# Kernel optimization log

Hardware: AMD Instinct MI355X
Metric: run time of the kernel (lower is better)

## Reference

```python
import jax, jax.numpy as jnp
import numpy as np

B, T, S, I, H = 128, 256, 256, 512, 512


def setup_inputs() -> dict:
    key = jax.random.key(0)
    ks = jax.random.split(key, 10)
    sc = 0.02
    return {
        "x": jax.random.normal(ks[0], (B, T, I), jnp.float32),
        "h0": jax.random.normal(ks[1], (B, H), jnp.float32),
        "c0": jax.random.normal(ks[2], (B, H), jnp.float32),
        "ctx": jax.random.normal(ks[3], (S, B, H), jnp.float32),
        "Wi": jax.random.normal(ks[4], (4 * H, I), jnp.float32) * sc,
        "bi": jax.random.normal(ks[5], (4 * H,), jnp.float32) * sc,
        "Wh": jax.random.normal(ks[6], (4 * H, H), jnp.float32) * sc,
        "bh": jax.random.normal(ks[7], (4 * H,), jnp.float32) * sc,
        "W_in": jax.random.normal(ks[8], (H, H), jnp.float32) * sc,
        "W_out": jax.random.normal(ks[9], (H, 2 * H), jnp.float32) * sc,
    }


def reference(x, h0, c0, ctx, Wi, bi, Wh, bh, W_in, W_out):
    ctx_b = jnp.transpose(ctx, (1, 0, 2))  # [B, S, H]

    def step(carry, xt):
        hx, cx = carry
        gates = xt @ Wi.T + bi + hx @ Wh.T + bh  # [B, 4H]
        i_g, f_g, g_g, o_g = jnp.split(gates, 4, axis=1)
        cy = jax.nn.sigmoid(f_g) * cx + jax.nn.sigmoid(i_g) * jnp.tanh(g_g)
        hy = jax.nn.sigmoid(o_g) * jnp.tanh(cy)
        # soft dot attention
        target = hy @ W_in.T                              # [B, H]
        attn = jax.nn.softmax(jnp.einsum('bsh,bh->bs', ctx_b, target), axis=1)
        wc = jnp.einsum('bs,bsh->bh', attn, ctx_b)        # [B, H]
        h_tilde = jnp.tanh(jnp.concatenate([wc, hy], axis=1) @ W_out.T)
        return (h_tilde, cy), h_tilde

    (hf, cf), outs = jax.lax.scan(step, (h0, c0), jnp.transpose(x, (1, 0, 2)))
    output = jnp.transpose(outs, (1, 0, 2))  # [B, T, H] (batch_first)
    return output, hf, cf
```

## Files before the change

kernel.cpp:

```cpp
#include <hip/hip_runtime.h>
#include <hip/hip_bf16.h>
#include <stdint.h>

#define B_ 128
#define T_ 256
#define S_ 256
#define I_ 512
#define H_ 512
#define RSLOT 32

typedef __attribute__((ext_vector_type(8))) short short8;
typedef __attribute__((ext_vector_type(4))) float f32x4;
typedef unsigned short ushort_t;
typedef unsigned long long u64;

__device__ __forceinline__ float bf2f(ushort_t u){
  union{ unsigned int i; float f;} v; v.i = ((unsigned int)u)<<16; return v.f;
}
__device__ __forceinline__ ushort_t f2bf(float f){
  union{ unsigned int i; float f;} v; v.f=f;
  unsigned int x=v.i; unsigned int r = x + 0x7fffu + ((x>>16)&1u);
  return (ushort_t)(r>>16);
}
__device__ __forceinline__ float sigm(float x){ return 1.f/(1.f + __expf(-x)); }
__device__ __forceinline__ float tanh_s(float x){
  float a = fabsf(x);
  float e = __expf(-2.f*a);
  float t = (1.f - e)/(1.f + e);
  return x < 0.f ? -t : t;
}

__device__ __forceinline__ f32x4 MFMA16(short8 a, short8 b, f32x4 c){
  typedef __attribute__((ext_vector_type(8))) __bf16 bf16x8;
  return __builtin_amdgcn_mfma_f32_16x16x32_bf16(
      __builtin_bit_cast(bf16x8, a), __builtin_bit_cast(bf16x8, b), c, 0, 0, 0);
}

__device__ __forceinline__ void fab_store_u64(void* p, u64 v){
  __hip_atomic_store((u64*)p, v, __ATOMIC_RELAXED, __HIP_MEMORY_SCOPE_AGENT);
}


__global__ void k_cvt_bf16(const float* __restrict__ src, ushort_t* __restrict__ dst, int n){
  int i = (blockIdx.x*blockDim.x + threadIdx.x)*4;
  int stride = gridDim.x*blockDim.x*4;
  for (; i < n; i += stride){
    float4 v = *(const float4*)(src + i);
    ushort4 o; o.x=f2bf(v.x); o.y=f2bf(v.y); o.z=f2bf(v.z); o.w=f2bf(v.w);
    *(ushort4*)(dst + i) = o;
  }
}

__global__ void k_init_state(const float* __restrict__ h0, const float* __restrict__ c0,
                             ushort_t* __restrict__ hring0, float* __restrict__ cyb){
  int i = blockIdx.x*blockDim.x + threadIdx.x;
  hring0[i] = f2bf(h0[i]);
  cyb[i] = c0[i];
}

__global__ void k_zero_bar(int* f){
  f[threadIdx.x] = 0;
}

__global__ __launch_bounds__(256) void k_gemm_bt(
    const float* __restrict__ A, const float* __restrict__ Bm,
    ushort_t* __restrict__ C, int M, int N, int K,
    const float* __restrict__ bias0, const float* __restrict__ bias1){
  __shared__ ushort_t Asm[128][40];
  __shared__ ushort_t Bsm[128][40];
  const int tid = threadIdx.x;
  const int mBase = blockIdx.x*128, nBase = blockIdx.y*128;
  const int l = tid & 63, wv = tid >> 6;
  const int wm = (wv>>1)*64, wn = (wv&1)*64;
  const int lr = l & 15, lq = l >> 4;
  const int srow = tid >> 1, scol = (tid & 1)*16;
  const float* Ap = A + (size_t)(mBase + srow)*K + scol;
  const float* Bp = Bm + (size_t)(nBase + srow)*K + scol;

  f32x4 acc[4][4];
  #pragma unroll
  for (int i=0;i<4;i++)
    #pragma unroll
    for (int j=0;j<4;j++) acc[i][j] = (f32x4)0.f;

  for (int k0 = 0; k0 < K; k0 += 32){
    float4 a0 = *(const float4*)(Ap + k0);
    float4 a1 = *(const float4*)(Ap + k0 + 4);
    float4 a2 = *(const float4*)(Ap + k0 + 8);
    float4 a3 = *(const float4*)(Ap + k0 + 12);
    float4 b0 = *(const float4*)(Bp + k0);
    float4 b1 = *(const float4*)(Bp + k0 + 4);
    float4 b2 = *(const float4*)(Bp + k0 + 8);
    float4 b3 = *(const float4*)(Bp + k0 + 12);
    __syncthreads();
    {
      ushort4 w;
      w.x=f2bf(a0.x); w.y=f2bf(a0.y); w.z=f2bf(a0.z); w.w=f2bf(a0.w);
      *(ushort4*)&Asm[srow][scol+0]  = w;
      w.x=f2bf(a1.x); w.y=f2bf(a1.y); w.z=f2bf(a1.z); w.w=f2bf(a1.w);
      *(ushort4*)&Asm[srow][scol+4]  = w;
      w.x=f2bf(a2.x); w.y=f2bf(a2.y); w.z=f2bf(a2.z); w.w=f2bf(a2.w);
      *(ushort4*)&Asm[srow][scol+8]  = w;
      w.x=f2bf(a3.x); w.y=f2bf(a3.y); w.z=f2bf(a3.z); w.w=f2bf(a3.w);
      *(ushort4*)&Asm[srow][scol+12] = w;
      w.x=f2bf(b0.x); w.y=f2bf(b0.y); w.z=f2bf(b0.z); w.w=f2bf(b0.w);
      *(ushort4*)&Bsm[srow][scol+0]  = w;
      w.x=f2bf(b1.x); w.y=f2bf(b1.y); w.z=f2bf(b1.z); w.w=f2bf(b1.w);
      *(ushort4*)&Bsm[srow][scol+4]  = w;
      w.x=f2bf(b2.x); w.y=f2bf(b2.y); w.z=f2bf(b2.z); w.w=f2bf(b2.w);
      *(ushort4*)&Bsm[srow][scol+8]  = w;
      w.x=f2bf(b3.x); w.y=f2bf(b3.y); w.z=f2bf(b3.z); w.w=f2bf(b3.w);
      *(ushort4*)&Bsm[srow][scol+12] = w;
    }
    __syncthreads();
    short8 aF[4], bF[4];
    #pragma unroll
    for (int i=0;i<4;i++) aF[i] = *(const short8*)&Asm[wm + i*16 + lr][lq*8];
    #pragma unroll
    for (int j=0;j<4;j++) bF[j] = *(const short8*)&Bsm[wn + j*16 + lr][lq*8];
    #pragma unroll
    for (int i=0;i<4;i++)
      #pragma unroll
      for (int j=0;j<4;j++)
        acc[i][j] = MFMA16(aF[i], bF[j], acc[i][j]);
  }

  #pragma unroll
  for (int j=0;j<4;j++){
    int col = nBase + wn + j*16 + lr;
    float bsum = bias0[col] + bias1[col];
    #pragma unroll
    for (int i=0;i<4;i++){
      int row0 = mBase + wm + i*16 + lq*4;
      #pragma unroll
      for (int r=0;r<4;r++)
        C[(size_t)(row0+r)*N + col] = f2bf(acc[i][j][r] + bsum);
    }
  }
}

__device__ __forceinline__ void gbar(int* flags, int gen){
  __syncthreads();
  const int tid = threadIdx.x;
  if (tid == 0)
    __hip_atomic_store(&flags[blockIdx.x], gen, __ATOMIC_RELAXED, __HIP_MEMORY_SCOPE_AGENT);
  if (tid < 256){
    while (__hip_atomic_load(&flags[tid], __ATOMIC_RELAXED, __HIP_MEMORY_SCOPE_AGENT) < gen)
      __builtin_amdgcn_s_sleep(2);
  }
  __syncthreads();
  asm volatile("" ::: "memory");
}


__global__ __launch_bounds__(512) void k_persist(
    const ushort_t* __restrict__ Xg, const float* __restrict__ ctx,
    const ushort_t* __restrict__ Whb, const ushort_t* __restrict__ Woutb,
    const ushort_t* __restrict__ Winb,
    ushort_t* hring, ushort_t* hyring, ushort_t* wcring,
    float* cyb, float* psmail, float* out, float* hf, float* cf,
    int* flags)
{
  extern __shared__ __align__(16) char ctx_s[];

  __shared__ __align__(16) union {
    struct { float red[8][256]; ushort_t pk[256]; } a;
    struct { float hy[512]; float tg[256]; float ps[256]; float sc[256];
             float p[256]; float inv; float pad;
             float pacc[16][256]; ushort_t pk[256]; } b;
  } sh;

  const int pbid = blockIdx.x;
  const int tid = threadIdx.x;
  const int l = tid & 63, wv = tid >> 6;
  const int lr = l & 15, lq = l >> 4;

  const int bm = pbid >> 5, hc = pbid & 31;
  const int gate = wv & 3, khalf = wv >> 2;
  short8 whr[8];
  #pragma unroll
  for (int kk=0;kk<8;kk++)
    whr[kk] = *(const short8*)(Whb + (size_t)(gate*512 + hc*16 + lr)*512
                               + khalf*256 + lq*8 + kk*32);
  short8 wor[4];
  #pragma unroll
  for (int kk=0;kk<4;kk++)
    wor[kk] = *(const short8*)(Woutb + (size_t)(hc*16 + lr)*1024
                               + wv*128 + lq*8 + kk*32);

  const int bB = pbid >> 1, half = pbid & 1;

  {
    const float* cp = ctx + (size_t)bB*512 + half*256 + (tid & 63)*4;
    #pragma unroll 4
    for (int i = 0; i < 32; ++i){
      int s = i*8 + (tid >> 6);
      float4 v = *(const float4*)(cp + (size_t)s*65536);
      ushort4 o; o.x=f2bf(v.x); o.y=f2bf(v.y); o.z=f2bf(v.z); o.w=f2bf(v.w);
      int boff = ((tid & 63)*8) ^ ((s & 7) << 4);
      *(ushort4*)(ctx_s + s*512 + boff) = o;
    }
  }
  __syncthreads();

  int gen = 0;
  for (int t = 0; t < T_; ++t){
    const size_t slotC = (size_t)(t & (RSLOT-1)) * 65536;
    const int slotI = t & (RSLOT-1);

    {
      ushort_t x0=0,x1=0,x2=0,x3=0; float co = 0.f;
      if (tid < 256){
        const int b = bm*16 + (tid>>4), h = hc*16 + (tid&15);
        const ushort_t* xg = Xg + ((size_t)b*T_ + t)*2048 + h;
        x0 = xg[0]; x1 = xg[512]; x2 = xg[1024]; x3 = xg[1536];
        co = cyb[b*512 + h];
      }
      f32x4 acc = (f32x4)0.f;
      const ushort_t* ap = hring + slotC + (size_t)(bm*16 + lr)*512 + khalf*256 + lq*8;
      short8 hv8[8];
      #pragma unroll
      for (int kk=0;kk<8;kk++) hv8[kk] = *(const short8*)(ap + kk*32);
      #pragma unroll
      for (int kk=0;kk<8;kk++) acc = MFMA16(hv8[kk], whr[kk], acc);
      #pragma unroll
      for (int r=0;r<4;r++) sh.a.red[wv][(lq*4+r)*16+lr] = acc[r];
      __syncthreads();
      if (tid < 256){
        const int b = bm*16 + (tid>>4), h = hc*16 + (tid&15);
        float gi  = sh.a.red[0][tid] + sh.a.red[4][tid] + bf2f(x0);
        float gf  = sh.a.red[1][tid] + sh.a.red[5][tid] + bf2f(x1);
        float gg  = sh.a.red[2][tid] + sh.a.red[6][tid] + bf2f(x2);
        float go_ = sh.a.red[3][tid] + sh.a.red[7][tid] + bf2f(x3);
        float cn = sigm(gf)*co + sigm(gi)*tanh_s(gg);
        float hn = sigm(go_)*tanh_s(cn);
        cyb[b*512 + h] = cn;
        sh.a.pk[tid] = f2bf(hn);
        if (t == T_-1) cf[b*512 + h] = cn;
      }
      __syncthreads();
      if (tid < 64){
        u64 v = *(u64*)&sh.a.pk[tid*4];
        fab_store_u64(hyring + slotC + (size_t)(bm*16 + (tid>>2))*512
                      + hc*16 + (tid&3)*4, v);
      }
    }
    gbar(flags, ++gen);

    {
      if (tid < 128){
        ushort4 v = *(const ushort4*)(hyring + slotC + (size_t)bB*512 + tid*4);
        sh.b.hy[tid*4+0]=bf2f(v.x); sh.b.hy[tid*4+1]=bf2f(v.y);
        sh.b.hy[tid*4+2]=bf2f(v.z); sh.b.hy[tid*4+3]=bf2f(v.w);
      }
      __syncthreads();
      {
        const int j = tid >> 1, kh = tid & 1;
        const ushort_t* wp = Winb + (size_t)(half*256 + j)*512 + kh*256;
        float d = 0.f;
        #pragma unroll
        for (int c = 0; c < 32; ++c){
          short8 w8 = *(const short8*)(wp + c*8);
          #pragma unroll
          for (int e=0;e<8;e++) d += bf2f((ushort_t)w8[e]) * sh.b.hy[kh*256 + c*8 + e];
        }
        d += __shfl_xor(d, 1);
        if (kh == 0) sh.b.tg[j] = d;
      }
      __syncthreads();
      {
        const int s = tid >> 1, qh = tid & 1;
        const int swz = (s & 7) << 4;
        float d = 0.f;
        #pragma unroll
        for (int c = 0; c < 16; ++c){
          int eb = c*16 + qh*8;
          short8 cv = *(const short8*)(ctx_s + s*512 + ((eb*2) ^ swz));
          #pragma unroll
          for (int e=0;e<8;e++) d += bf2f((ushort_t)cv[e]) * sh.b.tg[eb + e];
        }
        d += __shfl_xor(d, 1);
        if (qh == 0) sh.b.ps[s] = d;
      }
      __syncthreads();
      {
        float* mymail = psmail + ((size_t)(bB*2 + half)*RSLOT + slotI)*256;
        if (tid < 128)
          fab_store_u64(mymail + tid*2, *(u64*)&sh.b.ps[tid*2]);
      }
    }
    gbar(flags, ++gen);

    {
      {
        const float* budp = psmail + ((size_t)(bB*2 + (half^1))*RSLOT + slotI)*256;
        if (tid < 128){
          float2 f2 = *(const float2*)(budp + tid*2);
          sh.b.sc[tid*2]   = sh.b.ps[tid*2]   + f2.x;
          sh.b.sc[tid*2+1] = sh.b.ps[tid*2+1] + f2.y;
        }
      }
      __syncthreads();
      if (wv == 0){
        float v0=sh.b.sc[l], v1=sh.b.sc[l+64], v2=sh.b.sc[l+128], v3=sh.b.sc[l+192];
        float m = fmaxf(fmaxf(v0,v1), fmaxf(v2,v3));
        #pragma unroll
        for (int off=32; off; off>>=1) m = fmaxf(m, __shfl_xor(m, off));
        float e0=__expf(v0-m), e1=__expf(v1-m), e2=__expf(v2-m), e3=__expf(v3-m);
        float s4 = (e0+e1)+(e2+e3);
        #pragma unroll
        for (int off=32; off; off>>=1) s4 += __shfl_xor(s4, off);
        sh.b.p[l]=e0; sh.b.p[l+64]=e1; sh.b.p[l+128]=e2; sh.b.p[l+192]=e3;
        if (l==0) sh.b.inv = 1.f/s4;
      }
      __syncthreads();
      {
        const int g = tid & 31, p = tid >> 5;
        float a8[8];
        #pragma unroll
        for (int e=0;e<8;e++) a8[e]=0.f;
        #pragma unroll
        for (int j=0;j<16;j++){
          int s = p*16 + j;
          short8 cv = *(const short8*)(ctx_s + s*512 + ((g*16) ^ ((s&7)<<4)));
          float pw = sh.b.p[s];
          #pragma unroll
          for (int e=0;e<8;e++) a8[e] += pw * bf2f((ushort_t)cv[e]);
        }
        #pragma unroll
        for (int e=0;e<8;e++) sh.b.pacc[p][g*8+e] = a8[e];
      }
      __syncthreads();
      if (tid < 256){
        float ssum = 0.f;
        #pragma unroll
        for (int p2=0;p2<16;p2++) ssum += sh.b.pacc[p2][tid];
        sh.b.pk[tid] = f2bf(ssum * sh.b.inv);
      }
      __syncthreads();
      if (tid < 64){
        u64 v = *(u64*)&sh.b.pk[tid*4];
        fab_store_u64(wcring + slotC + (size_t)bB*512 + half*256 + tid*4, v);
      }
    }
    gbar(flags, ++gen);

    {
      f32x4 acc = (f32x4)0.f;
      const ushort_t* ap = (wv < 4 ? wcring : hyring) + slotC
                           + (size_t)(bm*16 + lr)*512 + (wv&3)*128 + lq*8;
      short8 av[4];
      #pragma unroll
      for (int kk=0;kk<4;kk++) av[kk] = *(const short8*)(ap + kk*32);
      #pragma unroll
      for (int kk=0;kk<4;kk++) acc = MFMA16(av[kk], wor[kk], acc);
      #pragma unroll
      for (int r=0;r<4;r++) sh.a.red[wv][(lq*4+r)*16+lr] = acc[r];
      __syncthreads();
      if (tid < 256){
        float s = 0.f;
        #pragma unroll
        for (int w=0;w<8;w++) s += sh.a.red[w][tid];
        float v = tanh_s(s);
        const int b = bm*16 + (tid>>4), n = hc*16 + (tid&15);
        out[((size_t)b*T_ + t)*512 + n] = v;
        sh.a.pk[tid] = f2bf(v);
        if (t == T_-1) hf[b*512 + n] = v;
      }
      __syncthreads();
      if (tid < 64){
        u64 v = *(u64*)&sh.a.pk[tid*4];
        size_t slotN = (size_t)((t+1) & (RSLOT-1)) * 65536;
        fab_store_u64(hring + slotN + (size_t)(bm*16 + (tid>>2))*512
                      + hc*16 + (tid&3)*4, v);
      }
    }
    gbar(flags, ++gen);
  }
}


extern "C" void kernel_launch(void* const* d_in, const int* in_sizes, int n_in,
                              void* d_out, int out_size, void* d_ws, size_t ws_size,
                              hipStream_t stream){
  const float* x    = (const float*)d_in[0];
  const float* h0   = (const float*)d_in[1];
  const float* c0   = (const float*)d_in[2];
  const float* ctx  = (const float*)d_in[3];
  const float* Wi   = (const float*)d_in[4];
  const float* bi   = (const float*)d_in[5];
  const float* Wh   = (const float*)d_in[6];
  const float* bh   = (const float*)d_in[7];
  const float* Win  = (const float*)d_in[8];
  const float* Wout = (const float*)d_in[9];

  char* ws = (char*)d_ws;
  ushort_t* Xg     = (ushort_t*)(ws);
  ushort_t* Whb    = (ushort_t*)(ws + 134217728);
  ushort_t* Woutb  = (ushort_t*)(ws + 136314880);
  ushort_t* Winb   = (ushort_t*)(ws + 137363456);
  ushort_t* hring  = (ushort_t*)(ws + 137887744);
  ushort_t* hyring = (ushort_t*)(ws + 142082048);
  ushort_t* wcring = (ushort_t*)(ws + 146276352);
  float*    cyb    = (float*)   (ws + 150470656);
  float*    psmail = (float*)   (ws + 150732800);
  int*      flags  = (int*)     (ws + 159121408);

  float* out = (float*)d_out;
  float* hf  = out + (size_t)B_*T_*H_;
  float* cf  = hf + (size_t)B_*H_;

  hipFuncSetAttribute((const void*)k_persist,
                      hipFuncAttributeMaxDynamicSharedMemorySize, 131072);

  k_cvt_bf16<<<512, 256, 0, stream>>>(Wh, Whb, 4*H_*H_);
  k_cvt_bf16<<<512, 256, 0, stream>>>(Wout, Woutb, H_*2*H_);
  k_cvt_bf16<<<256, 256, 0, stream>>>(Win, Winb, H_*H_);
  k_init_state<<<256, 256, 0, stream>>>(h0, c0, hring, cyb);
  k_zero_bar<<<1, 256, 0, stream>>>(flags);

  k_gemm_bt<<<dim3(256,16), 256, 0, stream>>>(x, Wi, Xg, B_*T_, 4*H_, I_, bi, bh);

  k_persist<<<256, 512, 131072, stream>>>(Xg, ctx, Whb, Woutb, Winb,
                                          hring, hyring, wcring,
                                          cyb, psmail, out, hf, cf,
                                          flags);
}
```

Baseline: 10.32 ms.

## Replace grid-wide barriers with tagged point-to-point data channels

Drops the four grid-wide flag barriers per timestep. In their place, each exchanged word carries a 32-bit step tag in the upper half of a 64-bit atomic, so consumers poll only the specific data they need (h, hy, partial scores, wc) instead of waiting for all 256 blocks. The change also interleaves the precomputed input-gate projection as [B,T,H,4] so one ushort4 load fetches all four gates, and it prefetches the next step's value. The cost is twice the bytes for every exchanged value, many more polling loads, and a 4-slot channel ring that relies on the dependency chain to prevent slot overwrite races.

After: 17.21 ms. 66.8% more time.

```diff
diff --git a/kernel.cpp b/kernel.cpp
--- a/kernel.cpp
+++ b/kernel.cpp
@@ -7,19 +7,20 @@
 #define S_ 256
 #define I_ 512
 #define H_ 512
-#define RSLOT 32
+#define CSLOT 4
 
 typedef __attribute__((ext_vector_type(8))) short short8;
 typedef __attribute__((ext_vector_type(4))) float f32x4;
 typedef unsigned short ushort_t;
 typedef unsigned long long u64;
+typedef unsigned int u32;
 
 __device__ __forceinline__ float bf2f(ushort_t u){
-  union{ unsigned int i; float f;} v; v.i = ((unsigned int)u)<<16; return v.f;
+  union{ u32 i; float f;} v; v.i = ((u32)u)<<16; return v.f;
 }
 __device__ __forceinline__ ushort_t f2bf(float f){
-  union{ unsigned int i; float f;} v; v.f=f;
-  unsigned int x=v.i; unsigned int r = x + 0x7fffu + ((x>>16)&1u);
+  union{ u32 i; float f;} v; v.f=f;
+  u32 x=v.i; u32 r = x + 0x7fffu + ((x>>16)&1u);
   return (ushort_t)(r>>16);
 }
 __device__ __forceinline__ float sigm(float x){ return 1.f/(1.f + __expf(-x)); }
@@ -36,8 +37,20 @@
       __builtin_bit_cast(bf16x8, a), __builtin_bit_cast(bf16x8, b), c, 0, 0, 0);
 }
 
-__device__ __forceinline__ void fab_store_u64(void* p, u64 v){
-  __hip_atomic_store((u64*)p, v, __ATOMIC_RELAXED, __HIP_MEMORY_SCOPE_AGENT);
+__device__ __forceinline__ void ch_st(u64* p, u32 tag, u32 payload){
+  __hip_atomic_store(p, ((u64)tag << 32) | payload,
+                     __ATOMIC_RELAXED, __HIP_MEMORY_SCOPE_AGENT);
+}
+__device__ __forceinline__ u64 ch_ld(const u64* p){
+  return __hip_atomic_load(p, __ATOMIC_RELAXED, __HIP_MEMORY_SCOPE_AGENT);
+}
+__device__ __forceinline__ u32 ch_poll(const u64* p, u32 tag){
+  u64 w = ch_ld(p);
+  while ((u32)(w >> 32) != tag){
+    __builtin_amdgcn_s_sleep(1);
+    w = ch_ld(p);
+  }
+  return (u32)w;
 }
 
 
@@ -51,15 +64,22 @@
   }
 }
 
+__global__ void k_zero_ch(u64* p, int n){
+  int i = blockIdx.x*blockDim.x + threadIdx.x;
+  if (i < n)
+    __hip_atomic_store(p + i, 0ull, __ATOMIC_RELAXED, __HIP_MEMORY_SCOPE_AGENT);
+}
+
 __global__ void k_init_state(const float* __restrict__ h0, const float* __restrict__ c0,
-                             ushort_t* __restrict__ hring0, float* __restrict__ cyb){
-  int i = blockIdx.x*blockDim.x + threadIdx.x;
-  hring0[i] = f2bf(h0[i]);
+                             u64* __restrict__ hCh, float* __restrict__ cyb){
+  int i = blockIdx.x*256 + threadIdx.x;
   cyb[i] = c0[i];
-}
-
-__global__ void k_zero_bar(int* f){
-  f[threadIdx.x] = 0;
+  if (i < 32768){
+    int b = i >> 8, w = i & 255;
+    u32 p = (u32)f2bf(h0[b*512 + w*2]) | ((u32)f2bf(h0[b*512 + w*2 + 1]) << 16);
+    __hip_atomic_store(hCh + i, ((u64)1 << 32) | p,
+                       __ATOMIC_RELAXED, __HIP_MEMORY_SCOPE_AGENT);
+  }
 }
 
 __global__ __launch_bounds__(256) void k_gemm_bt(
@@ -129,42 +149,29 @@
   for (int j=0;j<4;j++){
     int col = nBase + wn + j*16 + lr;
     float bsum = bias0[col] + bias1[col];
+    int h = col & 511, gatec = col >> 9;
     #pragma unroll
     for (int i=0;i<4;i++){
       int row0 = mBase + wm + i*16 + lq*4;
       #pragma unroll
       for (int r=0;r<4;r++)
-        C[(size_t)(row0+r)*N + col] = f2bf(acc[i][j][r] + bsum);
-    }
-  }
-}
-
-__device__ __forceinline__ void gbar(int* flags, int gen){
-  __syncthreads();
-  const int tid = threadIdx.x;
-  if (tid == 0)
-    __hip_atomic_store(&flags[blockIdx.x], gen, __ATOMIC_RELAXED, __HIP_MEMORY_SCOPE_AGENT);
-  if (tid < 256){
-    while (__hip_atomic_load(&flags[tid], __ATOMIC_RELAXED, __HIP_MEMORY_SCOPE_AGENT) < gen)
-      __builtin_amdgcn_s_sleep(2);
-  }
-  __syncthreads();
-  asm volatile("" ::: "memory");
+        C[((size_t)(row0+r)*512 + h)*4 + gatec] = f2bf(acc[i][j][r] + bsum);
+    }
+  }
 }
 
 
 __global__ __launch_bounds__(512) void k_persist(
-    const ushort_t* __restrict__ Xg, const float* __restrict__ ctx,
+    const ushort_t* __restrict__ Xg2, const float* __restrict__ ctx,
     const ushort_t* __restrict__ Whb, const ushort_t* __restrict__ Woutb,
     const ushort_t* __restrict__ Winb,
-    ushort_t* hring, ushort_t* hyring, ushort_t* wcring,
-    float* cyb, float* psmail, float* out, float* hf, float* cf,
-    int* flags)
+    u64* hCh, u64* hyCh, u64* wcCh, u64* psCh,
+    float* cyb, float* out, float* hf, float* cf)
 {
   extern __shared__ __align__(16) char ctx_s[];
 
   __shared__ __align__(16) union {
-    struct { float red[8][256]; ushort_t pk[256]; } a;
+    struct { float red[8][256]; ushort_t pk[256]; char hstage[16384]; } a;
     struct { float hy[512]; float tg[256]; float ps[256]; float sc[256];
              float p[256]; float inv; float pad;
              float pacc[16][256]; ushort_t pk[256]; } b;
@@ -189,6 +196,7 @@
                                + wv*128 + lq*8 + kk*32);
 
   const int bB = pbid >> 1, half = pbid & 1;
+  const int bA = bm*16 + ((tid & 255) >> 4), hA = hc*16 + (tid & 15);
 
   {
     const float* cp = ctx + (size_t)bB*512 + half*256 + (tid & 63)*4;
@@ -203,55 +211,73 @@
   }
   __syncthreads();
 
-  int gen = 0;
+  ushort4 xq_cur = make_ushort4(0,0,0,0), xq_next = make_ushort4(0,0,0,0);
+  if (tid < 256)
+    xq_cur = *(const ushort4*)(Xg2 + ((size_t)(bA*T_ + 0)*512 + hA)*4);
+
   for (int t = 0; t < T_; ++t){
-    const size_t slotC = (size_t)(t & (RSLOT-1)) * 65536;
-    const int slotI = t & (RSLOT-1);
+    const int slot = t & (CSLOT-1);
+    const u32 tg1 = (u32)(t + 1);
 
     {
-      ushort_t x0=0,x1=0,x2=0,x3=0; float co = 0.f;
-      if (tid < 256){
-        const int b = bm*16 + (tid>>4), h = hc*16 + (tid&15);
-        const ushort_t* xg = Xg + ((size_t)b*T_ + t)*2048 + h;
-        x0 = xg[0]; x1 = xg[512]; x2 = xg[1024]; x3 = xg[1536];
-        co = cyb[b*512 + h];
-      }
+      float co = 0.f;
+      if (tid < 256) co = cyb[bA*512 + hA];
+      {
+        const int r = tid >> 5, w8 = (tid & 31)*8;
+        const u64* hp = hCh + ((size_t)(slot*128 + bm*16 + r)*256) + w8;
+        u64 hw[8];
+        #pragma unroll
+        for (int j=0;j<8;j++) hw[j] = ch_ld(hp + j);
+        #pragma unroll
+        for (int j=0;j<8;j++){
+          while ((u32)(hw[j] >> 32) != tg1){
+            __builtin_amdgcn_s_sleep(1);
+            hw[j] = ch_ld(hp + j);
+          }
+        }
+        #pragma unroll
+        for (int j=0;j<8;j++)
+          *(u32*)(sh.a.hstage + r*1024 + ((((w8 + j)*4)) ^ ((r & 7) << 6))) = (u32)hw[j];
+      }
+      __syncthreads();
       f32x4 acc = (f32x4)0.f;
-      const ushort_t* ap = hring + slotC + (size_t)(bm*16 + lr)*512 + khalf*256 + lq*8;
-      short8 hv8[8];
-      #pragma unroll
-      for (int kk=0;kk<8;kk++) hv8[kk] = *(const short8*)(ap + kk*32);
-      #pragma unroll
-      for (int kk=0;kk<8;kk++) acc = MFMA16(hv8[kk], whr[kk], acc);
+      #pragma unroll
+      for (int kk=0;kk<8;kk++){
+        int u = khalf*512 + kk*64 + lq*16;
+        short8 aF = *(const short8*)(sh.a.hstage + lr*1024 + (u ^ ((lr & 7) << 6)));
+        acc = MFMA16(aF, whr[kk], acc);
+      }
       #pragma unroll
       for (int r=0;r<4;r++) sh.a.red[wv][(lq*4+r)*16+lr] = acc[r];
       __syncthreads();
       if (tid < 256){
-        const int b = bm*16 + (tid>>4), h = hc*16 + (tid&15);
-        float gi  = sh.a.red[0][tid] + sh.a.red[4][tid] + bf2f(x0);
-        float gf  = sh.a.red[1][tid] + sh.a.red[5][tid] + bf2f(x1);
-        float gg  = sh.a.red[2][tid] + sh.a.red[6][tid] + bf2f(x2);
-        float go_ = sh.a.red[3][tid] + sh.a.red[7][tid] + bf2f(x3);
+        float gi  = sh.a.red[0][tid] + sh.a.red[4][tid] + bf2f(xq_cur.x);
+        float gf  = sh.a.red[1][tid] + sh.a.red[5][tid] + bf2f(xq_cur.y);
+        float gg  = sh.a.red[2][tid] + sh.a.red[6][tid] + bf2f(xq_cur.z);
+        float go_ = sh.a.red[3][tid] + sh.a.red[7][tid] + bf2f(xq_cur.w);
         float cn = sigm(gf)*co + sigm(gi)*tanh_s(gg);
         float hn = sigm(go_)*tanh_s(cn);
-        cyb[b*512 + h] = cn;
+        cyb[bA*512 + hA] = cn;
         sh.a.pk[tid] = f2bf(hn);
-        if (t == T_-1) cf[b*512 + h] = cn;
-      }
-      __syncthreads();
-      if (tid < 64){
-        u64 v = *(u64*)&sh.a.pk[tid*4];
-        fab_store_u64(hyring + slotC + (size_t)(bm*16 + (tid>>2))*512
-                      + hc*16 + (tid&3)*4, v);
-      }
-    }
-    gbar(flags, ++gen);
+        if (t == T_-1) cf[bA*512 + hA] = cn;
+      }
+      __syncthreads();
+      if (tid < 128){
+        int r = tid >> 3, wi = tid & 7;
+        u32 p = (u32)sh.a.pk[r*16 + wi*2] | ((u32)sh.a.pk[r*16 + wi*2 + 1] << 16);
+        ch_st(hyCh + ((size_t)(slot*128 + bm*16 + r)*256) + hc*8 + wi, tg1, p);
+      }
+    }
 
     {
-      if (tid < 128){
-        ushort4 v = *(const ushort4*)(hyring + slotC + (size_t)bB*512 + tid*4);
-        sh.b.hy[tid*4+0]=bf2f(v.x); sh.b.hy[tid*4+1]=bf2f(v.y);
-        sh.b.hy[tid*4+2]=bf2f(v.z); sh.b.hy[tid*4+3]=bf2f(v.w);
+      if (tid < 256){
+        int tn = (t+1 < T_) ? t+1 : t;
+        xq_next = *(const ushort4*)(Xg2 + ((size_t)(bA*T_ + tn)*512 + hA)*4);
+      }
+      if (tid < 256){
+        u32 p = ch_poll(hyCh + ((size_t)(slot*128 + bB)*256) + tid, tg1);
+        sh.b.hy[tid*2]   = bf2f((ushort_t)(p & 0xffffu));
+        sh.b.hy[tid*2+1] = bf2f((ushort_t)(p >> 16));
       }
       __syncthreads();
       {
@@ -283,22 +309,15 @@
         if (qh == 0) sh.b.ps[s] = d;
       }
       __syncthreads();
-      {
-        float* mymail = psmail + ((size_t)(bB*2 + half)*RSLOT + slotI)*256;
-        if (tid < 128)
-          fab_store_u64(mymail + tid*2, *(u64*)&sh.b.ps[tid*2]);
-      }
-    }
-    gbar(flags, ++gen);
+      if (tid < 256)
+        ch_st(psCh + (((size_t)(slot*128 + bB)*2 + half)*256) + tid,
+              tg1, __builtin_bit_cast(u32, sh.b.ps[tid]));
+    }
 
     {
-      {
-        const float* budp = psmail + ((size_t)(bB*2 + (half^1))*RSLOT + slotI)*256;
-        if (tid < 128){
-          float2 f2 = *(const float2*)(budp + tid*2);
-          sh.b.sc[tid*2]   = sh.b.ps[tid*2]   + f2.x;
-          sh.b.sc[tid*2+1] = sh.b.ps[tid*2+1] + f2.y;
-        }
+      if (tid < 256){
+        u32 p = ch_poll(psCh + (((size_t)(slot*128 + bB)*2 + (half^1))*256) + tid, tg1);
+        sh.b.sc[tid] = sh.b.ps[tid] + __builtin_bit_cast(float, p);
       }
       __syncthreads();
       if (wv == 0){
@@ -315,20 +334,20 @@
       }
       __syncthreads();
       {
-        const int g = tid & 31, p = tid >> 5;
+        const int g = tid & 31, p2 = tid >> 5;
         float a8[8];
         #pragma unroll
         for (int e=0;e<8;e++) a8[e]=0.f;
         #pragma unroll
         for (int j=0;j<16;j++){
-          int s = p*16 + j;
+          int s = p2*16 + j;
           short8 cv = *(const short8*)(ctx_s + s*512 + ((g*16) ^ ((s&7)<<4)));
           float pw = sh.b.p[s];
           #pragma unroll
           for (int e=0;e<8;e++) a8[e] += pw * bf2f((ushort_t)cv[e]);
         }
         #pragma unroll
-        for (int e=0;e<8;e++) sh.b.pacc[p][g*8+e] = a8[e];
+        for (int e=0;e<8;e++) sh.b.pacc[p2][g*8+e] = a8[e];
       }
       __syncthreads();
       if (tid < 256){
@@ -338,44 +357,55 @@
         sh.b.pk[tid] = f2bf(ssum * sh.b.inv);
       }
       __syncthreads();
-      if (tid < 64){
-        u64 v = *(u64*)&sh.b.pk[tid*4];
-        fab_store_u64(wcring + slotC + (size_t)bB*512 + half*256 + tid*4, v);
-      }
-    }
-    gbar(flags, ++gen);
+      if (tid < 128)
+        ch_st(wcCh + ((size_t)(slot*128 + bB)*256) + half*128 + tid,
+              tg1, (u32)sh.b.pk[tid*2] | ((u32)sh.b.pk[tid*2+1] << 16));
+    }
 
     {
+      const u64* chb = (wv < 4) ? wcCh : hyCh;
+      const u64* cp0 = chb + ((size_t)(slot*128 + bm*16 + lr)*256) + (wv&3)*64 + lq*4;
+      u64 w[16];
+      #pragma unroll
+      for (int kk=0;kk<4;kk++)
+        #pragma unroll
+        for (int j=0;j<4;j++) w[kk*4+j] = ch_ld(cp0 + kk*16 + j);
+      #pragma unroll
+      for (int i=0;i<16;i++){
+        while ((u32)(w[i] >> 32) != tg1){
+          __builtin_amdgcn_s_sleep(1);
+          w[i] = ch_ld(cp0 + (i>>2)*16 + (i&3));
+        }
+      }
       f32x4 acc = (f32x4)0.f;
-      const ushort_t* ap = (wv < 4 ? wcring : hyring) + slotC
-                           + (size_t)(bm*16 + lr)*512 + (wv&3)*128 + lq*8;
-      short8 av[4];
-      #pragma unroll
-      for (int kk=0;kk<4;kk++) av[kk] = *(const short8*)(ap + kk*32);
-      #pragma unroll
-      for (int kk=0;kk<4;kk++) acc = MFMA16(av[kk], wor[kk], acc);
+      #pragma unroll
+      for (int kk=0;kk<4;kk++){
+        int4 q;
+        q.x = (int)(u32)w[kk*4+0]; q.y = (int)(u32)w[kk*4+1];
+        q.z = (int)(u32)w[kk*4+2]; q.w = (int)(u32)w[kk*4+3];
+        acc = MFMA16(__builtin_bit_cast(short8, q), wor[kk], acc);
+      }
       #pragma unroll
       for (int r=0;r<4;r++) sh.a.red[wv][(lq*4+r)*16+lr] = acc[r];
       __syncthreads();
       if (tid < 256){
         float s = 0.f;
         #pragma unroll
-        for (int w=0;w<8;w++) s += sh.a.red[w][tid];
+        for (int w8=0;w8<8;w8++) s += sh.a.red[w8][tid];
         float v = tanh_s(s);
-        const int b = bm*16 + (tid>>4), n = hc*16 + (tid&15);
-        out[((size_t)b*T_ + t)*512 + n] = v;
+        out[((size_t)bA*T_ + t)*512 + hA] = v;
         sh.a.pk[tid] = f2bf(v);
-        if (t == T_-1) hf[b*512 + n] = v;
-      }
-      __syncthreads();
-      if (tid < 64){
-        u64 v = *(u64*)&sh.a.pk[tid*4];
-        size_t slotN = (size_t)((t+1) & (RSLOT-1)) * 65536;
-        fab_store_u64(hring + slotN + (size_t)(bm*16 + (tid>>2))*512
-                      + hc*16 + (tid&3)*4, v);
-      }
-    }
-    gbar(flags, ++gen);
+        if (t == T_-1) hf[bA*512 + hA] = v;
+      }
+      __syncthreads();
+      if (tid < 128){
+        int r = tid >> 3, wi = tid & 7;
+        u32 p = (u32)sh.a.pk[r*16 + wi*2] | ((u32)sh.a.pk[r*16 + wi*2 + 1] << 16);
+        ch_st(hCh + ((size_t)(((t+1) & (CSLOT-1))*128 + bm*16 + r)*256) + hc*8 + wi,
+              (u32)(t + 2), p);
+      }
+    }
+    xq_cur = xq_next;
   }
 }
 
@@ -395,16 +425,15 @@
   const float* Wout = (const float*)d_in[9];
 
   char* ws = (char*)d_ws;
-  ushort_t* Xg     = (ushort_t*)(ws);
-  ushort_t* Whb    = (ushort_t*)(ws + 134217728);
-  ushort_t* Woutb  = (ushort_t*)(ws + 136314880);
-  ushort_t* Winb   = (ushort_t*)(ws + 137363456);
-  ushort_t* hring  = (ushort_t*)(ws + 137887744);
-  ushort_t* hyring = (ushort_t*)(ws + 142082048);
-  ushort_t* wcring = (ushort_t*)(ws + 146276352);
-  float*    cyb    = (float*)   (ws + 150470656);
-  float*    psmail = (float*)   (ws + 150732800);
-  int*      flags  = (int*)     (ws + 159121408);
+  ushort_t* Xg2   = (ushort_t*)(ws);
+  ushort_t* Whb   = (ushort_t*)(ws + 134217728);
+  ushort_t* Woutb = (ushort_t*)(ws + 136314880);
+  ushort_t* Winb  = (ushort_t*)(ws + 137363456);
+  u64*      hyCh  = (u64*)     (ws + 137887744);
+  u64*      hCh   = (u64*)     (ws + 138936320);
+  u64*      wcCh  = (u64*)     (ws + 139984896);
+  u64*      psCh  = (u64*)     (ws + 141033472);
+  float*    cyb   = (float*)   (ws + 143130624);
 
   float* out = (float*)d_out;
   float* hf  = out + (size_t)B_*T_*H_;
@@ -413,16 +442,16 @@
   hipFuncSetAttribute((const void*)k_persist,
                       hipFuncAttributeMaxDynamicSharedMemorySize, 131072);
 
+  k_zero_ch<<<2560, 256, 0, stream>>>(hyCh, 655360);
+  k_init_state<<<256, 256, 0, stream>>>(h0, c0, hCh, cyb);
+
   k_cvt_bf16<<<512, 256, 0, stream>>>(Wh, Whb, 4*H_*H_);
   k_cvt_bf16<<<512, 256, 0, stream>>>(Wout, Woutb, H_*2*H_);
   k_cvt_bf16<<<256, 256, 0, stream>>>(Win, Winb, H_*H_);
-  k_init_state<<<256, 256, 0, stream>>>(h0, c0, hring, cyb);
-  k_zero_bar<<<1, 256, 0, stream>>>(flags);
-
-  k_gemm_bt<<<dim3(256,16), 256, 0, stream>>>(x, Wi, Xg, B_*T_, 4*H_, I_, bi, bh);
-
-  k_persist<<<256, 512, 131072, stream>>>(Xg, ctx, Whb, Woutb, Winb,
-                                          hring, hyring, wcring,
-                                          cyb, psmail, out, hf, cf,
-                                          flags);
-}
+
+  k_gemm_bt<<<dim3(256,16), 256, 0, stream>>>(x, Wi, Xg2, B_*T_, 4*H_, I_, bi, bh);
+
+  k_persist<<<256, 512, 131072, stream>>>(Xg2, ctx, Whb, Woutb, Winb,
+                                          hCh, hyCh, wcCh, psCh,
+                                          cyb, out, hf, cf);
+}
```

## Split attention over sequence halves with flash-style merge, cut one grid barrier per step

Applied to the files above, without the earlier changes.

Each block now holds half of the source positions, with full hidden width, for one batch row. It computes the target projection and a local softmax with partial weighted context, then publishes the partial sums and its max/sum pair. The partner block merges the two halves online-softmax style and computes the output projection directly with SIMT dot products. This removes the score-mailbox exchange and the separate MFMA output stage, saving one grid-wide barrier per timestep. It also interleaves the input-gate layout so the four gates load as one vector and prefetches the next step's gates. The trade-off is more scalar FMA work per block, since W_in and W_out are now read from global memory each step with no MFMA.

Measured after the change: 16.71 ms. 61.9% more time.

```diff
diff --git a/kernel.cpp b/kernel.cpp
--- a/kernel.cpp
+++ b/kernel.cpp
@@ -13,13 +13,14 @@
 typedef __attribute__((ext_vector_type(4))) float f32x4;
 typedef unsigned short ushort_t;
 typedef unsigned long long u64;
+typedef unsigned int u32;
 
 __device__ __forceinline__ float bf2f(ushort_t u){
-  union{ unsigned int i; float f;} v; v.i = ((unsigned int)u)<<16; return v.f;
+  union{ u32 i; float f;} v; v.i = ((u32)u)<<16; return v.f;
 }
 __device__ __forceinline__ ushort_t f2bf(float f){
-  union{ unsigned int i; float f;} v; v.f=f;
-  unsigned int x=v.i; unsigned int r = x + 0x7fffu + ((x>>16)&1u);
+  union{ u32 i; float f;} v; v.f=f;
+  u32 x=v.i; u32 r = x + 0x7fffu + ((x>>16)&1u);
   return (ushort_t)(r>>16);
 }
 __device__ __forceinline__ float sigm(float x){ return 1.f/(1.f + __expf(-x)); }
@@ -59,7 +60,7 @@
 }
 
 __global__ void k_zero_bar(int* f){
-  f[threadIdx.x] = 0;
+  if (threadIdx.x < 256) f[threadIdx.x] = 0;
 }
 
 __global__ __launch_bounds__(256) void k_gemm_bt(
@@ -129,12 +130,13 @@
   for (int j=0;j<4;j++){
     int col = nBase + wn + j*16 + lr;
     float bsum = bias0[col] + bias1[col];
+    int h = col & 511, gatec = col >> 9;
     #pragma unroll
     for (int i=0;i<4;i++){
       int row0 = mBase + wm + i*16 + lq*4;
       #pragma unroll
       for (int r=0;r<4;r++)
-        C[(size_t)(row0+r)*N + col] = f2bf(acc[i][j][r] + bsum);
+        C[((size_t)(row0+r)*512 + h)*4 + gatec] = f2bf(acc[i][j][r] + bsum);
     }
   }
 }
@@ -154,20 +156,20 @@
 
 
 __global__ __launch_bounds__(512) void k_persist(
-    const ushort_t* __restrict__ Xg, const float* __restrict__ ctx,
+    const ushort_t* __restrict__ Xg2, const float* __restrict__ ctx,
     const ushort_t* __restrict__ Whb, const ushort_t* __restrict__ Woutb,
     const ushort_t* __restrict__ Winb,
-    ushort_t* hring, ushort_t* hyring, ushort_t* wcring,
-    float* cyb, float* psmail, float* out, float* hf, float* cf,
+    ushort_t* hring, ushort_t* hyring, ushort_t* wcpring, float* mlring,
+    float* cyb, float* out, float* hf, float* cf,
     int* flags)
 {
   extern __shared__ __align__(16) char ctx_s[];
 
   __shared__ __align__(16) union {
     struct { float red[8][256]; ushort_t pk[256]; } a;
-    struct { float hy[512]; float tg[256]; float ps[256]; float sc[256];
-             float p[256]; float inv; float pad;
-             float pacc[16][256]; ushort_t pk[256]; } b;
+    struct { float hy[512]; float tg[512]; float sc[128]; float p[128];
+             float mo, lo;
+             float pacc[8][512]; float wcpm[512]; float wc[512]; ushort_t pk[256]; } b;
   } sh;
 
   const int pbid = blockIdx.x;
@@ -182,26 +184,25 @@
   for (int kk=0;kk<8;kk++)
     whr[kk] = *(const short8*)(Whb + (size_t)(gate*512 + hc*16 + lr)*512
                                + khalf*256 + lq*8 + kk*32);
-  short8 wor[4];
-  #pragma unroll
-  for (int kk=0;kk<4;kk++)
-    wor[kk] = *(const short8*)(Woutb + (size_t)(hc*16 + lr)*1024
-                               + wv*128 + lq*8 + kk*32);
-
   const int bB = pbid >> 1, half = pbid & 1;
+  const int bA = bm*16 + ((tid & 255) >> 4), hA = hc*16 + (tid & 15);
 
   {
-    const float* cp = ctx + (size_t)bB*512 + half*256 + (tid & 63)*4;
+    const int c4 = (tid & 127)*4;
     #pragma unroll 4
     for (int i = 0; i < 32; ++i){
-      int s = i*8 + (tid >> 6);
-      float4 v = *(const float4*)(cp + (size_t)s*65536);
+      int s_loc = i*4 + (tid >> 7);
+      float4 v = *(const float4*)(ctx + (((size_t)(half*128 + s_loc)*128 + bB)*512) + c4);
       ushort4 o; o.x=f2bf(v.x); o.y=f2bf(v.y); o.z=f2bf(v.z); o.w=f2bf(v.w);
-      int boff = ((tid & 63)*8) ^ ((s & 7) << 4);
-      *(ushort4*)(ctx_s + s*512 + boff) = o;
+      int boff = (c4*2) ^ ((s_loc & 7) << 4);
+      *(ushort4*)(ctx_s + s_loc*1024 + boff) = o;
     }
   }
   __syncthreads();
+
+  ushort4 xq_cur = make_ushort4(0,0,0,0), xq_next = make_ushort4(0,0,0,0);
+  if (tid < 256)
+    xq_cur = *(const ushort4*)(Xg2 + ((size_t)(bA*T_ + 0)*512 + hA)*4);
 
   int gen = 0;
   for (int t = 0; t < T_; ++t){
@@ -209,13 +210,8 @@
     const int slotI = t & (RSLOT-1);
 
     {
-      ushort_t x0=0,x1=0,x2=0,x3=0; float co = 0.f;
-      if (tid < 256){
-        const int b = bm*16 + (tid>>4), h = hc*16 + (tid&15);
-        const ushort_t* xg = Xg + ((size_t)b*T_ + t)*2048 + h;
-        x0 = xg[0]; x1 = xg[512]; x2 = xg[1024]; x3 = xg[1536];
-        co = cyb[b*512 + h];
-      }
+      float co = 0.f;
+      if (tid < 256) co = cyb[bA*512 + hA];
       f32x4 acc = (f32x4)0.f;
       const ushort_t* ap = hring + slotC + (size_t)(bm*16 + lr)*512 + khalf*256 + lq*8;
       short8 hv8[8];
@@ -227,16 +223,15 @@
       for (int r=0;r<4;r++) sh.a.red[wv][(lq*4+r)*16+lr] = acc[r];
       __syncthreads();
       if (tid < 256){
-        const int b = bm*16 + (tid>>4), h = hc*16 + (tid&15);
-        float gi  = sh.a.red[0][tid] + sh.a.red[4][tid] + bf2f(x0);
-        float gf  = sh.a.red[1][tid] + sh.a.red[5][tid] + bf2f(x1);
-        float gg  = sh.a.red[2][tid] + sh.a.red[6][tid] + bf2f(x2);
-        float go_ = sh.a.red[3][tid] + sh.a.red[7][tid] + bf2f(x3);
+        float gi  = sh.a.red[0][tid] + sh.a.red[4][tid] + bf2f(xq_cur.x);
+        float gf  = sh.a.red[1][tid] + sh.a.red[5][tid] + bf2f(xq_cur.y);
+        float gg  = sh.a.red[2][tid] + sh.a.red[6][tid] + bf2f(xq_cur.z);
+        float go_ = sh.a.red[3][tid] + sh.a.red[7][tid] + bf2f(xq_cur.w);
         float cn = sigm(gf)*co + sigm(gi)*tanh_s(gg);
         float hn = sigm(go_)*tanh_s(cn);
-        cyb[b*512 + h] = cn;
+        cyb[bA*512 + hA] = cn;
         sh.a.pk[tid] = f2bf(hn);
-        if (t == T_-1) cf[b*512 + h] = cn;
+        if (t == T_-1) cf[bA*512 + hA] = cn;
       }
       __syncthreads();
       if (tid < 64){
@@ -248,6 +243,10 @@
     gbar(flags, ++gen);
 
     {
+      if (tid < 256){
+        int tn = (t+1 < T_) ? t+1 : t;
+        xq_next = *(const ushort4*)(Xg2 + ((size_t)(bA*T_ + tn)*512 + hA)*4);
+      }
       if (tid < 128){
         ushort4 v = *(const ushort4*)(hyring + slotC + (size_t)bB*512 + tid*4);
         sh.b.hy[tid*4+0]=bf2f(v.x); sh.b.hy[tid*4+1]=bf2f(v.y);
@@ -255,127 +254,124 @@
       }
       __syncthreads();
       {
-        const int j = tid >> 1, kh = tid & 1;
-        const ushort_t* wp = Winb + (size_t)(half*256 + j)*512 + kh*256;
+        const ushort_t* wp = Winb + (size_t)tid*512;
         float d = 0.f;
-        #pragma unroll
-        for (int c = 0; c < 32; ++c){
+        #pragma unroll 8
+        for (int c = 0; c < 64; ++c){
           short8 w8 = *(const short8*)(wp + c*8);
           #pragma unroll
-          for (int e=0;e<8;e++) d += bf2f((ushort_t)w8[e]) * sh.b.hy[kh*256 + c*8 + e];
+          for (int e=0;e<8;e++) d += bf2f((ushort_t)w8[e]) * sh.b.hy[c*8 + e];
+        }
+        sh.b.tg[tid] = d;
+      }
+      __syncthreads();
+      {
+        const int s_loc = tid >> 2, q4 = tid & 3;
+        const int swz = (s_loc & 7) << 4;
+        float d = 0.f;
+        #pragma unroll
+        for (int c = 0; c < 16; ++c){
+          int hb = q4*256 + c*16;
+          short8 cv = *(const short8*)(ctx_s + s_loc*1024 + (hb ^ swz));
+          #pragma unroll
+          for (int e=0;e<8;e++) d += bf2f((ushort_t)cv[e]) * sh.b.tg[q4*128 + c*8 + e];
         }
         d += __shfl_xor(d, 1);
-        if (kh == 0) sh.b.tg[j] = d;
-      }
-      __syncthreads();
-      {
-        const int s = tid >> 1, qh = tid & 1;
-        const int swz = (s & 7) << 4;
-        float d = 0.f;
-        #pragma unroll
-        for (int c = 0; c < 16; ++c){
-          int eb = c*16 + qh*8;
-          short8 cv = *(const short8*)(ctx_s + s*512 + ((eb*2) ^ swz));
-          #pragma unroll
-          for (int e=0;e<8;e++) d += bf2f((ushort_t)cv[e]) * sh.b.tg[eb + e];
-        }
-        d += __shfl_xor(d, 1);
-        if (qh == 0) sh.b.ps[s] = d;
-      }
-      __syncthreads();
-      {
-        float* mymail = psmail + ((size_t)(bB*2 + half)*RSLOT + slotI)*256;
-        if (tid < 128)
-          fab_store_u64(mymail + tid*2, *(u64*)&sh.b.ps[tid*2]);
-      }
-    }
-    gbar(flags, ++gen);
-
-    {
-      {
-        const float* budp = psmail + ((size_t)(bB*2 + (half^1))*RSLOT + slotI)*256;
-        if (tid < 128){
-          float2 f2 = *(const float2*)(budp + tid*2);
-          sh.b.sc[tid*2]   = sh.b.ps[tid*2]   + f2.x;
-          sh.b.sc[tid*2+1] = sh.b.ps[tid*2+1] + f2.y;
-        }
+        d += __shfl_xor(d, 2);
+        if (q4 == 0) sh.b.sc[s_loc] = d;
       }
       __syncthreads();
       if (wv == 0){
-        float v0=sh.b.sc[l], v1=sh.b.sc[l+64], v2=sh.b.sc[l+128], v3=sh.b.sc[l+192];
-        float m = fmaxf(fmaxf(v0,v1), fmaxf(v2,v3));
+        float v0 = sh.b.sc[l], v1 = sh.b.sc[l+64];
+        float m = fmaxf(v0, v1);
         #pragma unroll
         for (int off=32; off; off>>=1) m = fmaxf(m, __shfl_xor(m, off));
-        float e0=__expf(v0-m), e1=__expf(v1-m), e2=__expf(v2-m), e3=__expf(v3-m);
-        float s4 = (e0+e1)+(e2+e3);
-        #pragma unroll
-        for (int off=32; off; off>>=1) s4 += __shfl_xor(s4, off);
-        sh.b.p[l]=e0; sh.b.p[l+64]=e1; sh.b.p[l+128]=e2; sh.b.p[l+192]=e3;
-        if (l==0) sh.b.inv = 1.f/s4;
-      }
-      __syncthreads();
-      {
-        const int g = tid & 31, p = tid >> 5;
+        float e0 = __expf(v0 - m), e1 = __expf(v1 - m);
+        float s2 = e0 + e1;
+        #pragma unroll
+        for (int off=32; off; off>>=1) s2 += __shfl_xor(s2, off);
+        sh.b.p[l] = e0; sh.b.p[l+64] = e1;
+        if (l == 0){ sh.b.mo = m; sh.b.lo = s2; }
+      }
+      __syncthreads();
+      {
+        const int strip = tid >> 6, hg = tid & 63;
         float a8[8];
         #pragma unroll
         for (int e=0;e<8;e++) a8[e]=0.f;
         #pragma unroll
-        for (int j=0;j<16;j++){
-          int s = p*16 + j;
-          short8 cv = *(const short8*)(ctx_s + s*512 + ((g*16) ^ ((s&7)<<4)));
-          float pw = sh.b.p[s];
+        for (int j = 0; j < 16; ++j){
+          int s_loc = strip*16 + j;
+          short8 cv = *(const short8*)(ctx_s + s_loc*1024 + ((hg*16) ^ ((s_loc&7)<<4)));
+          float pw = sh.b.p[s_loc];
           #pragma unroll
           for (int e=0;e<8;e++) a8[e] += pw * bf2f((ushort_t)cv[e]);
         }
         #pragma unroll
-        for (int e=0;e<8;e++) sh.b.pacc[p][g*8+e] = a8[e];
-      }
-      __syncthreads();
-      if (tid < 256){
-        float ssum = 0.f;
-        #pragma unroll
-        for (int p2=0;p2<16;p2++) ssum += sh.b.pacc[p2][tid];
-        sh.b.pk[tid] = f2bf(ssum * sh.b.inv);
+        for (int e=0;e<8;e++) sh.b.pacc[strip][hg*8+e] = a8[e];
+      }
+      __syncthreads();
+      {
+        float s = 0.f;
+        #pragma unroll
+        for (int st=0;st<8;st++) s += sh.b.pacc[st][tid];
+        sh.b.wcpm[tid] = s;
+      }
+      __syncthreads();
+      if (tid < 128){
+        ushort4 w;
+        w.x = f2bf(sh.b.wcpm[tid*4+0]); w.y = f2bf(sh.b.wcpm[tid*4+1]);
+        w.z = f2bf(sh.b.wcpm[tid*4+2]); w.w = f2bf(sh.b.wcpm[tid*4+3]);
+        fab_store_u64(wcpring + (((size_t)(slotI*128 + bB)*2 + half)*512) + tid*4,
+                      __builtin_bit_cast(u64, w));
+      }
+      if (tid == 128){
+        float2 ml = make_float2(sh.b.mo, sh.b.lo);
+        fab_store_u64(mlring + (((size_t)(slotI*128 + bB)*2 + half)*2),
+                      __builtin_bit_cast(u64, ml));
+      }
+    }
+    gbar(flags, ++gen);
+
+    {
+      float2 mlp = *(const float2*)(mlring + (((size_t)(slotI*128 + bB)*2 + (half^1))*2));
+      float m  = fmaxf(sh.b.mo, mlp.x);
+      float ao = __expf(sh.b.mo - m), ap_ = __expf(mlp.x - m);
+      float inv = 1.f / (ao*sh.b.lo + ap_*mlp.y);
+      {
+        const ushort_t* wpp = wcpring + (((size_t)(slotI*128 + bB)*2 + (half^1))*512);
+        sh.b.wc[tid] = (ao*sh.b.wcpm[tid] + ap_*bf2f(wpp[tid])) * inv;
+      }
+      __syncthreads();
+      {
+        const int j2 = tid >> 1, kh = tid & 1;
+        const int n = half*256 + j2;
+        const ushort_t* wp = Woutb + (size_t)n*1024 + kh*512;
+        const float* src = kh ? sh.b.hy : sh.b.wc;
+        float d = 0.f;
+        #pragma unroll 8
+        for (int c = 0; c < 64; ++c){
+          short8 w8 = *(const short8*)(wp + c*8);
+          #pragma unroll
+          for (int e=0;e<8;e++) d += bf2f((ushort_t)w8[e]) * src[c*8 + e];
+        }
+        d += __shfl_xor(d, 1);
+        if (kh == 0){
+          float v = tanh_s(d);
+          out[((size_t)bB*T_ + t)*512 + n] = v;
+          sh.b.pk[j2] = f2bf(v);
+          if (t == T_-1) hf[bB*512 + n] = v;
+        }
       }
       __syncthreads();
       if (tid < 64){
         u64 v = *(u64*)&sh.b.pk[tid*4];
-        fab_store_u64(wcring + slotC + (size_t)bB*512 + half*256 + tid*4, v);
+        size_t slotN = (size_t)((t+1) & (RSLOT-1)) * 65536;
+        fab_store_u64(hring + slotN + (size_t)bB*512 + half*256 + tid*4, v);
       }
     }
     gbar(flags, ++gen);
-
-    {
-      f32x4 acc = (f32x4)0.f;
-      const ushort_t* ap = (wv < 4 ? wcring : hyring) + slotC
-                           + (size_t)(bm*16 + lr)*512 + (wv&3)*128 + lq*8;
-      short8 av[4];
-      #pragma unroll
-      for (int kk=0;kk<4;kk++) av[kk] = *(const short8*)(ap + kk*32);
-      #pragma unroll
-      for (int kk=0;kk<4;kk++) acc = MFMA16(av[kk], wor[kk], acc);
-      #pragma unroll
-      for (int r=0;r<4;r++) sh.a.red[wv][(lq*4+r)*16+lr] = acc[r];
-      __syncthreads();
-      if (tid < 256){
-        float s = 0.f;
-        #pragma unroll
-        for (int w=0;w<8;w++) s += sh.a.red[w][tid];
-        float v = tanh_s(s);
-        const int b = bm*16 + (tid>>4), n = hc*16 + (tid&15);
-        out[((size_t)b*T_ + t)*512 + n] = v;
-        sh.a.pk[tid] = f2bf(v);
-        if (t == T_-1) hf[b*512 + n] = v;
-      }
-      __syncthreads();
-      if (tid < 64){
-        u64 v = *(u64*)&sh.a.pk[tid*4];
-        size_t slotN = (size_t)((t+1) & (RSLOT-1)) * 65536;
-        fab_store_u64(hring + slotN + (size_t)(bm*16 + (tid>>2))*512
-                      + hc*16 + (tid&3)*4, v);
-      }
-    }
-    gbar(flags, ++gen);
+    xq_cur = xq_next;
   }
 }
 
@@ -395,16 +391,16 @@
   const float* Wout = (const float*)d_in[9];
 
   char* ws = (char*)d_ws;
-  ushort_t* Xg     = (ushort_t*)(ws);
-  ushort_t* Whb    = (ushort_t*)(ws + 134217728);
-  ushort_t* Woutb  = (ushort_t*)(ws + 136314880);
-  ushort_t* Winb   = (ushort_t*)(ws + 137363456);
-  ushort_t* hring  = (ushort_t*)(ws + 137887744);
-  ushort_t* hyring = (ushort_t*)(ws + 142082048);
-  ushort_t* wcring = (ushort_t*)(ws + 146276352);
-  float*    cyb    = (float*)   (ws + 150470656);
-  float*    psmail = (float*)   (ws + 150732800);
-  int*      flags  = (int*)     (ws + 159121408);
+  ushort_t* Xg2     = (ushort_t*)(ws);
+  ushort_t* Whb     = (ushort_t*)(ws + 134217728);
+  ushort_t* Woutb   = (ushort_t*)(ws + 136314880);
+  ushort_t* Winb    = (ushort_t*)(ws + 137363456);
+  ushort_t* hring   = (ushort_t*)(ws + 137887744);
+  ushort_t* hyring  = (ushort_t*)(ws + 142082048);
+  ushort_t* wcpring = (ushort_t*)(ws + 146276352);
+  float*    mlring  = (float*)   (ws + 154664960);
+  float*    cyb     = (float*)   (ws + 154730496);
+  int*      flags   = (int*)     (ws + 154992640);
 
   float* out = (float*)d_out;
   float* hf  = out + (size_t)B_*T_*H_;
@@ -413,16 +409,17 @@
   hipFuncSetAttribute((const void*)k_persist,
                       hipFuncAttributeMaxDynamicSharedMemorySize, 131072);
 
+  k_zero_bar<<<1, 256, 0, stream>>>(flags);
+  k_init_state<<<256, 256, 0, stream>>>(h0, c0, hring, cyb);
+
   k_cvt_bf16<<<512, 256, 0, stream>>>(Wh, Whb, 4*H_*H_);
   k_cvt_bf16<<<512, 256, 0, stream>>>(Wout, Woutb, H_*2*H_);
   k_cvt_bf16<<<256, 256, 0, stream>>>(Win, Winb, H_*H_);
-  k_init_state<<<256, 256, 0, stream>>>(h0, c0, hring, cyb);
-  k_zero_bar<<<1, 256, 0, stream>>>(flags);
-
-  k_gemm_bt<<<dim3(256,16), 256, 0, stream>>>(x, Wi, Xg, B_*T_, 4*H_, I_, bi, bh);
-
-  k_persist<<<256, 512, 131072, stream>>>(Xg, ctx, Whb, Woutb, Winb,
-                                          hring, hyring, wcring,
-                                          cyb, psmail, out, hf, cf,
+
+  k_gemm_bt<<<dim3(256,16), 256, 0, stream>>>(x, Wi, Xg2, B_*T_, 4*H_, I_, bi, bh);
+
+  k_persist<<<256, 512, 131072, stream>>>(Xg2, ctx, Whb, Woutb, Winb,
+                                          hring, hyring, wcpring, mlring,
+                                          cyb, out, hf, cf,
                                           flags);
 }
```
